# Optimization experiments

Measured on AMD Instinct MI355X. Metric: run time of the kernel, lower is better.

## Reference

```python
import jax, jax.numpy as jnp
import numpy as np

B, TQ, TK, D, F, H = 16, 256, 256, 256, 36, 8
DK = D // H          # dk = d // h
SF = int(np.sqrt(F)) # 6
MASK_VALUE = -1e30


def setup_inputs() -> dict:
    rng = jax.random.key(0)
    ks = jax.random.split(rng, 12)
    s = 0.05
    return {
        "query": jax.random.normal(ks[0], (B, TQ, D), jnp.float32),
        "key_ts": jax.random.normal(ks[1], (B, TK, D), jnp.float32),
        "value": jax.random.normal(ks[2], (B, TK, F), jnp.float32),
        "mask": (jax.random.uniform(ks[3], (B, TK, F)) < 0.5).astype(jnp.float32),
        "Wq": jax.random.normal(ks[4], (H, D, DK), jnp.float32) * s,
        "Wk": jax.random.normal(ks[5], (H, D, DK), jnp.float32) * s,
        "Wc": jax.random.normal(ks[6], (H, D), jnp.float32) * s,
        "bc": jnp.zeros((D,), jnp.float32),
        "Wo_1": jax.random.normal(ks[7], (F, SF), jnp.float32) * s,
        "bo_1": jnp.zeros((SF,), jnp.float32),
        "Wo_2": jax.random.normal(ks[8], (SF, 1), jnp.float32) * s,
        "bo_2": jnp.zeros((D,), jnp.float32),
    }


def reference(query, key_ts, value, mask, Wq, Wk, Wc, bc, Wo_1, bo_1, Wo_2, bo_2):
    # mask: [B, Tk, F] 0/1 missingness indicator -> broadcast as [B, 1, Tk, F]
    m = mask[:, None, :, :]
    heads = []
    for j in range(Wq.shape[0]):  # fixed small head loop (h=8)
        q = query @ Wq[j]                                  # [B, Tq, dk]
        k = key_ts @ Wk[j]                                 # [B, Tk, dk]
        A = jnp.einsum('bqd,bkd->bqk', q, k)[..., None]    # [B, Tq, Tk, 1] (no 1/sqrt(dk) scaling, as in original)
        A = m * A + (1.0 - m) * MASK_VALUE                 # [B, Tq, Tk, F]
        A = jax.nn.softmax(A, axis=-2)                     # softmax over Tk, per feature
        heads.append(jnp.einsum('bqkf,bkf->bqf', A, value))  # masked weighted sum
    latent = jnp.stack(heads, axis=-1)                     # [B, Tq, F, h]
    # permute (0,2,1,3) -> [B, F, Tq, h]; dot Wc[h,d] -> [B, F, Tq, d]
    latent = jnp.tanh(jnp.einsum('bqfh,hd->bfqd', latent, Wc) + bc)
    # permute (0,2,3,1) -> [B, Tq, d, F]; Wo_1: F -> sqrt(F)
    x = jnp.tanh(jnp.einsum('bfqd,fs->bqds', latent, Wo_1) + bo_1)
    # Wo_2: sqrt(F) -> 1, squeeze, add bo_2 -> [B, Tq, d]
    x = jnp.einsum('bqds,so->bqd', x, Wo_2) + bo_2
    return x
```

## Files before the change

kernel.cpp:

```cpp
#include <hip/hip_runtime.h>

#define NB 16
#define NTQ 256
#define NTK 256
#define ND 256
#define NF 36
#define NH 8
#define NDK 32
#define NSF 6

typedef __attribute__((ext_vector_type(8))) short short8;
typedef __attribute__((ext_vector_type(4))) float f32x4;
#define MFMA16(a,b,c) __builtin_amdgcn_mfma_f32_16x16x32_bf16(a,b,c,0,0,0)

#define SZ_QP  (16*8*256*32*2)
#define QPH_OFF 0
#define QPL_OFF (QPH_OFF + SZ_QP)
#define KPH_OFF (QPL_OFF + SZ_QP)
#define KPL_OFF (KPH_OFF + SZ_QP)
#define SZ_RT  (16*80*256*2)
#define RT_OFF  (KPL_OFF + SZ_QP)
#define HD_OFF  (RT_OFF + SZ_RT)

__device__ __forceinline__ short f2bf(float x){
    union { float f; unsigned u; } v; v.f = x;
    unsigned r = v.u + 0x7fffu + ((v.u >> 16) & 1u);
    return (short)(r >> 16);
}
__device__ __forceinline__ float bf2f(short s){
    union { float f; unsigned u; } v; v.u = ((unsigned)(unsigned short)s) << 16;
    return v.f;
}
__device__ __forceinline__ float fast_tanh(float x){
    float e = __expf(2.0f*x);
    return 1.0f - 2.0f/(e + 1.0f);
}
__device__ __forceinline__ short8 ld8(const short* p){ return *(const short8*)p; }

__device__ __forceinline__ void cvt8(const float* __restrict__ p, short8& h8, short8& l8){
    f32x4 a = *(const f32x4*)p;
    f32x4 c = *(const f32x4*)(p + 4);
    #pragma unroll
    for (int i = 0; i < 4; ++i){
        short h0 = f2bf(a[i]); h8[i]   = h0; l8[i]   = f2bf(a[i] - bf2f(h0));
        short h1 = f2bf(c[i]); h8[4+i] = h1; l8[4+i] = f2bf(c[i] - bf2f(h1));
    }
}

__global__ void imta_prep(const float* __restrict__ query, const float* __restrict__ key_ts,
                          const float* __restrict__ Wq, const float* __restrict__ Wk,
                          const float* __restrict__ mask, const float* __restrict__ value,
                          char* __restrict__ wsb){
    if (blockIdx.y == 2){
        const int b = blockIdx.z, k = threadIdx.x;
        short* rt = (short*)(wsb + RT_OFF) + b*80*256;
        #pragma unroll
        for (int r = 0; r < 5; ++r){
            const int fp = blockIdx.x*5 + r;
            const int f = fp >> 1;
            short o = 0;
            if (f < NF){
                float m = mask[(b*NTK + k)*NF + f];
                o = (fp & 1) ? f2bf(m) : f2bf(m * value[(b*NTK + k)*NF + f]);
            }
            rt[fp*256 + k] = o;
        }
        return;
    }
    const int side = blockIdx.y, b = blockIdx.z;
    const int mt = blockIdx.x >> 1, nh = blockIdx.x & 1;
    const int t0 = mt*32;
    const int tid = threadIdx.x, w = tid >> 6, lane = tid & 63;
    const int col = lane & 15, quad = lane >> 4;
    const float* __restrict__ X = side ? key_ts : query;
    const float* __restrict__ W = side ? Wk : Wq;
    __shared__ float sX[32][36];
    __shared__ float sW[128][36];
    const int xr = tid >> 3, xc = (tid & 7)*4;
    const int dr = tid >> 3, dkq = (tid & 7)*4;
    f32x4 acc[2][2];
    #pragma unroll
    for (int m = 0; m < 2; ++m){ acc[m][0] = (f32x4)0.f; acc[m][1] = (f32x4)0.f; }
    for (int kb = 0; kb < 8; ++kb){
        const int dc = kb*32;
        float4 xv = *(const float4*)(X + (size_t)(b*NTQ + t0 + xr)*ND + dc + xc);
        float4 wv[4];
        #pragma unroll
        for (int jj = 0; jj < 4; ++jj)
            wv[jj] = *(const float4*)(W + (size_t)((4*nh + jj)*ND + dc + dr)*NDK + dkq);
        __syncthreads();
        *(float4*)&sX[xr][xc] = xv;
        #pragma unroll
        for (int jj = 0; jj < 4; ++jj)
            #pragma unroll
            for (int i = 0; i < 4; ++i)
                sW[jj*32 + dkq + i][dr] = ((const float*)&wv[jj])[i];
        __syncthreads();
        short8 ah[2], al[2], bh[2], bl[2];
        #pragma unroll
        for (int m = 0; m < 2; ++m)
            cvt8(&sX[m*16 + col][quad*8], ah[m], al[m]);
        #pragma unroll
        for (int nt = 0; nt < 2; ++nt)
            cvt8(&sW[(w*2 + nt)*16 + col][quad*8], bh[nt], bl[nt]);
        #pragma unroll
        for (int m = 0; m < 2; ++m)
            #pragma unroll
            for (int nt = 0; nt < 2; ++nt){
                acc[m][nt] = MFMA16(al[m], bh[nt], acc[m][nt]);
                acc[m][nt] = MFMA16(ah[m], bl[nt], acc[m][nt]);
                acc[m][nt] = MFMA16(ah[m], bh[nt], acc[m][nt]);
            }
    }
    short* oh = (short*)(wsb + (side ? KPH_OFF : QPH_OFF));
    short* ol = (short*)(wsb + (side ? KPL_OFF : QPL_OFF));
    #pragma unroll
    for (int m = 0; m < 2; ++m)
        #pragma unroll
        for (int nt = 0; nt < 2; ++nt){
            const int n = (nh*8 + w*2 + nt)*16 + col;
            const int j = n >> 5, dk = n & 31;
            #pragma unroll
            for (int r = 0; r < 4; ++r){
                const int t = t0 + m*16 + quad*4 + r;
                float v = acc[m][nt][r];
                short h = f2bf(v);
                size_t o = (size_t)(((b*NH + j)*NTQ + t)*NDK + dk);
                oh[o] = h; ol[o] = f2bf(v - bf2f(h));
            }
        }
}

__global__ void imta_attn(char* __restrict__ wsb, const float* __restrict__ value){
    const int t0 = blockIdx.x*64;
    const int j = blockIdx.y, b = blockIdx.z;
    const int tid = threadIdx.x, w = tid >> 6, lane = tid & 63;
    const int col = lane & 15, quad = lane >> 4;
    __shared__ short sE[64*264];
    const short* QH = (const short*)(wsb + QPH_OFF) + (b*NH + j)*NTQ*NDK;
    const short* QL = (const short*)(wsb + QPL_OFF) + (b*NH + j)*NTQ*NDK;
    const short* KH = (const short*)(wsb + KPH_OFF) + (b*NH + j)*NTK*NDK;
    const short* KL = (const short*)(wsb + KPL_OFF) + (b*NH + j)*NTK*NDK;
    const short* RT = (const short*)(wsb + RT_OFF) + b*80*256;
    float* HD = (float*)(wsb + HD_OFF) + (b*NH + j)*NTQ*NF;

    short8 ah[4], al[4];
    #pragma unroll
    for (int m = 0; m < 4; ++m){
        const int t = t0 + m*16 + col;
        ah[m] = ld8(QH + t*NDK + quad*8);
        al[m] = ld8(QL + t*NDK + quad*8);
    }
    #pragma unroll
    for (int nt = 0; nt < 4; ++nt){
        const int key0 = w*64 + nt*16;
        short8 bh = ld8(KH + (key0 + col)*NDK + quad*8);
        short8 bl = ld8(KL + (key0 + col)*NDK + quad*8);
        f32x4 acc[4];
        #pragma unroll
        for (int m = 0; m < 4; ++m){
            f32x4 c = (f32x4)0.f;
            c = MFMA16(al[m], bh, c);
            c = MFMA16(ah[m], bl, c);
            c = MFMA16(ah[m], bh, c);
            acc[m] = c;
        }
        const int key = key0 + col;
        #pragma unroll
        for (int m = 0; m < 4; ++m)
            #pragma unroll
            for (int r = 0; r < 4; ++r){
                const int q = m*16 + quad*4 + r;
                sE[q*264 + key] = f2bf(__expf(acc[m][r]));
            }
    }
    __syncthreads();

    const int q0 = w*16;
    f32x4 acc2[5];
    #pragma unroll
    for (int nt = 0; nt < 5; ++nt) acc2[nt] = (f32x4)0.f;
    #pragma unroll 2
    for (int kb = 0; kb < 8; ++kb){
        const int ko = kb*32 + quad*8;
        short8 a = *(const short8*)&sE[(q0 + col)*264 + ko];
        #pragma unroll
        for (int nt = 0; nt < 5; ++nt){
            short8 bb = ld8(RT + (nt*16 + col)*256 + ko);
            acc2[nt] = MFMA16(a, bb, acc2[nt]);
        }
    }
    __syncthreads();
    float* sH = (float*)sE;
    #pragma unroll
    for (int nt = 0; nt < 5; ++nt)
        #pragma unroll
        for (int r = 0; r < 4; ++r){
            float v = acc2[nt][r];
            float o = __shfl_xor(v, 1, 64);
            if (!(col & 1)){
                const int f = nt*8 + (col >> 1);
                if (f < NF){
                    float num = v, den = o, h;
                    if (den != 0.0f) h = num/den;
                    else {
                        float s = 0.f;
                        for (int k = 0; k < NTK; ++k) s += value[(b*NTK + k)*NF + f];
                        h = s * (1.0f/256.0f);
                    }
                    sH[(q0 + quad*4 + r)*40 + f] = h;
                }
            }
        }
    __syncthreads();
    for (int idx = tid; idx < 64*NF; idx += 256){
        const int q = idx/NF, f = idx - q*NF;
        HD[(t0 + q)*NF + f] = sH[q*40 + f];
    }
}

__global__ void imta_final(const float* __restrict__ Wc, const float* __restrict__ bc,
                           const float* __restrict__ Wo1, const float* __restrict__ bo1,
                           const float* __restrict__ Wo2, const float* __restrict__ bo2,
                           const float* __restrict__ hd, float* __restrict__ out){
    const int bq = blockIdx.x;
    const int b = bq >> 8, qq = bq & 255;
    const int tid = threadIdx.x;
    __shared__ float sh[NF*NH];
    __shared__ float sW1[NF*NSF];
    for (int t = tid; t < NF*NH; t += 256){
        int jj = t/NF, f = t - jj*NF;
        sh[t] = hd[((b*NH + jj)*NTQ + qq)*NF + f];
    }
    if (tid < NF*NSF) sW1[tid] = Wo1[tid];
    __syncthreads();
    const int d = tid;
    float wcr[8];
    #pragma unroll
    for (int h = 0; h < 8; ++h) wcr[h] = Wc[h*ND + d];
    const float bcd = bc[d];
    float a2[6];
    #pragma unroll
    for (int s = 0; s < 6; ++s) a2[s] = bo1[s];
    #pragma unroll
    for (int f4 = 0; f4 < NF; f4 += 4){
        float4 sv[8];
        #pragma unroll
        for (int h = 0; h < 8; ++h) sv[h] = *(const float4*)&sh[h*NF + f4];
        #pragma unroll
        for (int fi = 0; fi < 4; ++fi){
            float a = bcd;
            #pragma unroll
            for (int h = 0; h < 8; ++h)
                a = fmaf(reinterpret_cast<const float*>(&sv[h])[fi], wcr[h], a);
            float lf = fast_tanh(a);
            const int f = f4 + fi;
            #pragma unroll
            for (int s = 0; s < 6; ++s)
                a2[s] = fmaf(lf, sW1[f*NSF + s], a2[s]);
        }
    }
    float o = bo2[d];
    #pragma unroll
    for (int s = 0; s < 6; ++s)
        o = fmaf(fast_tanh(a2[s]), Wo2[s], o);
    out[(b*NTQ + qq)*ND + d] = o;
}

extern "C" void kernel_launch(void* const* d_in, const int* in_sizes, int n_in,
                              void* d_out, int out_size, void* d_ws, size_t ws_size,
                              hipStream_t stream){
    const float* query  = (const float*)d_in[0];
    const float* key_ts = (const float*)d_in[1];
    const float* value  = (const float*)d_in[2];
    const float* mask   = (const float*)d_in[3];
    const float* Wq     = (const float*)d_in[4];
    const float* Wk     = (const float*)d_in[5];
    const float* Wc     = (const float*)d_in[6];
    const float* bc     = (const float*)d_in[7];
    const float* Wo1    = (const float*)d_in[8];
    const float* bo1    = (const float*)d_in[9];
    const float* Wo2    = (const float*)d_in[10];
    const float* bo2    = (const float*)d_in[11];
    char* wsb  = (char*)d_ws;
    float* out = (float*)d_out;
    (void)in_sizes; (void)n_in; (void)out_size; (void)ws_size;

    imta_prep <<<dim3(16, 3, 16), dim3(256), 0, stream>>>(query, key_ts, Wq, Wk, mask, value, wsb);
    imta_attn <<<dim3(4, 8, 16),  dim3(256), 0, stream>>>(wsb, value);
    imta_final<<<dim3(4096),      dim3(256), 0, stream>>>(Wc, bc, Wo1, bo1, Wo2, bo2,
                                                          (const float*)(wsb + HD_OFF), out);
}
```

Before: 143.0 us.

## Fuse Q/K head projections into attention kernel, prepack inputs to split-bf16

The prep kernel no longer computes the Q and K projections. It now only converts query, key_ts and the transposed Wq/Wk into hi/lo bf16 pairs, plus the mask/value RT table. Each attention block computes its own K projection for all 256 keys and the Q projection for its 64 queries with split-bf16 MFMA, staging the results in shared memory before scores. This removes the projected-Q/K round trip through global memory and the separate projection pass. The cost is that K is recomputed once per query tile (4x redundancy) and attention blocks get longer and heavier on registers.

```diff
diff --git a/kernel.cpp b/kernel.cpp
--- a/kernel.cpp
+++ b/kernel.cpp
@@ -13,14 +13,16 @@
 typedef __attribute__((ext_vector_type(4))) float f32x4;
 #define MFMA16(a,b,c) __builtin_amdgcn_mfma_f32_16x16x32_bf16(a,b,c,0,0,0)
 
-#define SZ_QP  (16*8*256*32*2)
-#define QPH_OFF 0
-#define QPL_OFF (QPH_OFF + SZ_QP)
-#define KPH_OFF (QPL_OFF + SZ_QP)
-#define KPL_OFF (KPH_OFF + SZ_QP)
-#define SZ_RT  (16*80*256*2)
-#define RT_OFF  (KPL_OFF + SZ_QP)
-#define HD_OFF  (RT_OFF + SZ_RT)
+#define QXH_OFF 0u
+#define QXL_OFF  (2u*1024*1024)
+#define KXH_OFF  (4u*1024*1024)
+#define KXL_OFF  (6u*1024*1024)
+#define WQTH_OFF (8u*1024*1024)
+#define WQTL_OFF (WQTH_OFF + 131072u)
+#define WKTH_OFF (WQTH_OFF + 262144u)
+#define WKTL_OFF (WQTH_OFF + 393216u)
+#define RT_OFF   (WQTH_OFF + 524288u)
+#define HD_OFF   (RT_OFF + 655360u)
 
 __device__ __forceinline__ short f2bf(float x){
     union { float f; unsigned u; } v; v.f = x;
@@ -47,135 +49,185 @@
     }
 }
 
-__global__ void imta_prep(const float* __restrict__ query, const float* __restrict__ key_ts,
+__global__ void imta_pack(const float* __restrict__ query, const float* __restrict__ key_ts,
                           const float* __restrict__ Wq, const float* __restrict__ Wk,
                           const float* __restrict__ mask, const float* __restrict__ value,
                           char* __restrict__ wsb){
-    if (blockIdx.y == 2){
-        const int b = blockIdx.z, k = threadIdx.x;
-        short* rt = (short*)(wsb + RT_OFF) + b*80*256;
-        #pragma unroll
-        for (int r = 0; r < 5; ++r){
-            const int fp = blockIdx.x*5 + r;
-            const int f = fp >> 1;
-            short o = 0;
-            if (f < NF){
-                float m = mask[(b*NTK + k)*NF + f];
-                o = (fp & 1) ? f2bf(m) : f2bf(m * value[(b*NTK + k)*NF + f]);
-            }
-            rt[fp*256 + k] = o;
-        }
+    const int bid = blockIdx.x, tid = threadIdx.x;
+    if (bid < 1024){
+        const int half = bid >> 9;
+        const float* __restrict__ X = half ? key_ts : query;
+        short* oh = (short*)(wsb + (half ? KXH_OFF : QXH_OFF));
+        short* ol = (short*)(wsb + (half ? KXL_OFF : QXL_OFF));
+        const int e = ((bid & 511)*256 + tid)*8;
+        short8 h8, l8;
+        cvt8(X + e, h8, l8);
+        *(short8*)(oh + e) = h8;
+        *(short8*)(ol + e) = l8;
         return;
     }
-    const int side = blockIdx.y, b = blockIdx.z;
-    const int mt = blockIdx.x >> 1, nh = blockIdx.x & 1;
-    const int t0 = mt*32;
-    const int tid = threadIdx.x, w = tid >> 6, lane = tid & 63;
-    const int col = lane & 15, quad = lane >> 4;
-    const float* __restrict__ X = side ? key_ts : query;
-    const float* __restrict__ W = side ? Wk : Wq;
-    __shared__ float sX[32][36];
-    __shared__ float sW[128][36];
-    const int xr = tid >> 3, xc = (tid & 7)*4;
-    const int dr = tid >> 3, dkq = (tid & 7)*4;
-    f32x4 acc[2][2];
-    #pragma unroll
-    for (int m = 0; m < 2; ++m){ acc[m][0] = (f32x4)0.f; acc[m][1] = (f32x4)0.f; }
-    for (int kb = 0; kb < 8; ++kb){
-        const int dc = kb*32;
-        float4 xv = *(const float4*)(X + (size_t)(b*NTQ + t0 + xr)*ND + dc + xc);
-        float4 wv[4];
-        #pragma unroll
-        for (int jj = 0; jj < 4; ++jj)
-            wv[jj] = *(const float4*)(W + (size_t)((4*nh + jj)*ND + dc + dr)*NDK + dkq);
-        __syncthreads();
-        *(float4*)&sX[xr][xc] = xv;
-        #pragma unroll
-        for (int jj = 0; jj < 4; ++jj)
-            #pragma unroll
-            for (int i = 0; i < 4; ++i)
-                sW[jj*32 + dkq + i][dr] = ((const float*)&wv[jj])[i];
-        __syncthreads();
-        short8 ah[2], al[2], bh[2], bl[2];
-        #pragma unroll
-        for (int m = 0; m < 2; ++m)
-            cvt8(&sX[m*16 + col][quad*8], ah[m], al[m]);
-        #pragma unroll
-        for (int nt = 0; nt < 2; ++nt)
-            cvt8(&sW[(w*2 + nt)*16 + col][quad*8], bh[nt], bl[nt]);
-        #pragma unroll
-        for (int m = 0; m < 2; ++m)
-            #pragma unroll
-            for (int nt = 0; nt < 2; ++nt){
-                acc[m][nt] = MFMA16(al[m], bh[nt], acc[m][nt]);
-                acc[m][nt] = MFMA16(ah[m], bl[nt], acc[m][nt]);
-                acc[m][nt] = MFMA16(ah[m], bh[nt], acc[m][nt]);
-            }
-    }
-    short* oh = (short*)(wsb + (side ? KPH_OFF : QPH_OFF));
-    short* ol = (short*)(wsb + (side ? KPL_OFF : QPL_OFF));
-    #pragma unroll
-    for (int m = 0; m < 2; ++m)
-        #pragma unroll
-        for (int nt = 0; nt < 2; ++nt){
-            const int n = (nh*8 + w*2 + nt)*16 + col;
-            const int j = n >> 5, dk = n & 31;
-            #pragma unroll
-            for (int r = 0; r < 4; ++r){
-                const int t = t0 + m*16 + quad*4 + r;
-                float v = acc[m][nt][r];
-                short h = f2bf(v);
-                size_t o = (size_t)(((b*NH + j)*NTQ + t)*NDK + dk);
-                oh[o] = h; ol[o] = f2bf(v - bf2f(h));
-            }
-        }
-}
-
-__global__ void imta_attn(char* __restrict__ wsb, const float* __restrict__ value){
+    if (bid < 1536){
+        const int idx = (bid - 1024)*256 + tid;
+        const int arr = idx >> 16, rem = idx & 65535;
+        const int d = rem & 255, jdk = rem >> 8;
+        const int jj = jdk >> 5, dk = jdk & 31;
+        const float* __restrict__ W = arr ? Wk : Wq;
+        float v = W[(jj*ND + d)*NDK + dk];
+        short h = f2bf(v);
+        short* oh = (short*)(wsb + (arr ? WKTH_OFF : WQTH_OFF));
+        short* ol = (short*)(wsb + (arr ? WKTL_OFF : WQTL_OFF));
+        oh[rem] = h; ol[rem] = f2bf(v - bf2f(h));
+        return;
+    }
+    const int rb = bid - 1536;
+    const int x = rb & 15, b = rb >> 4;
+    const int k = tid;
+    short* rt = (short*)(wsb + RT_OFF) + b*80*256;
+    #pragma unroll
+    for (int r = 0; r < 5; ++r){
+        const int fp = x*5 + r;
+        const int f = fp >> 1;
+        short o = 0;
+        if (f < NF){
+            float m = mask[(b*NTK + k)*NF + f];
+            o = (fp & 1) ? f2bf(m) : f2bf(m * value[(b*NTK + k)*NF + f]);
+        }
+        rt[fp*256 + k] = o;
+    }
+}
+
+__global__ __launch_bounds__(256, 2)
+void imta_attn(char* __restrict__ wsb, const float* __restrict__ value){
     const int t0 = blockIdx.x*64;
     const int j = blockIdx.y, b = blockIdx.z;
     const int tid = threadIdx.x, w = tid >> 6, lane = tid & 63;
     const int col = lane & 15, quad = lane >> 4;
-    __shared__ short sE[64*264];
-    const short* QH = (const short*)(wsb + QPH_OFF) + (b*NH + j)*NTQ*NDK;
-    const short* QL = (const short*)(wsb + QPL_OFF) + (b*NH + j)*NTQ*NDK;
-    const short* KH = (const short*)(wsb + KPH_OFF) + (b*NH + j)*NTK*NDK;
-    const short* KL = (const short*)(wsb + KPL_OFF) + (b*NH + j)*NTK*NDK;
-    const short* RT = (const short*)(wsb + RT_OFF) + b*80*256;
-    float* HD = (float*)(wsb + HD_OFF) + (b*NH + j)*NTQ*NF;
-
-    short8 ah[4], al[4];
-    #pragma unroll
-    for (int m = 0; m < 4; ++m){
-        const int t = t0 + m*16 + col;
-        ah[m] = ld8(QH + t*NDK + quad*8);
-        al[m] = ld8(QL + t*NDK + quad*8);
-    }
-    #pragma unroll
-    for (int nt = 0; nt < 4; ++nt){
-        const int key0 = w*64 + nt*16;
-        short8 bh = ld8(KH + (key0 + col)*NDK + quad*8);
-        short8 bl = ld8(KL + (key0 + col)*NDK + quad*8);
-        f32x4 acc[4];
+
+    __shared__ short sBuf[20480];
+    short* const sKH = sBuf;
+    short* const sKL = sBuf + 8192;
+    short* const sQH = sBuf + 16384;
+    short* const sQL = sBuf + 18432;
+
+    const short* KXH = (const short*)(wsb + KXH_OFF) + (size_t)b*NTK*ND;
+    const short* KXL = (const short*)(wsb + KXL_OFF) + (size_t)b*NTK*ND;
+    const short* QXH = (const short*)(wsb + QXH_OFF) + (size_t)b*NTQ*ND;
+    const short* QXL = (const short*)(wsb + QXL_OFF) + (size_t)b*NTQ*ND;
+    const short* WKH = (const short*)(wsb + WKTH_OFF) + j*NDK*ND;
+    const short* WKL = (const short*)(wsb + WKTL_OFF) + j*NDK*ND;
+    const short* WQH = (const short*)(wsb + WQTH_OFF) + j*NDK*ND;
+    const short* WQL = (const short*)(wsb + WQTL_OFF) + j*NDK*ND;
+
+    {
+        f32x4 kacc[4][2];
+        #pragma unroll
+        for (int mt = 0; mt < 4; ++mt){ kacc[mt][0] = (f32x4)0.f; kacc[mt][1] = (f32x4)0.f; }
+        #pragma unroll
+        for (int kb = 0; kb < 8; ++kb){
+            const int dko = kb*32 + quad*8;
+            short8 wbh[2], wbl[2];
+            #pragma unroll
+            for (int nb = 0; nb < 2; ++nb){
+                wbh[nb] = ld8(WKH + (nb*16 + col)*ND + dko);
+                wbl[nb] = ld8(WKL + (nb*16 + col)*ND + dko);
+            }
+            #pragma unroll
+            for (int mt = 0; mt < 4; ++mt){
+                const int krow = w*64 + mt*16 + col;
+                short8 ah = ld8(KXH + krow*ND + dko);
+                short8 al = ld8(KXL + krow*ND + dko);
+                #pragma unroll
+                for (int nb = 0; nb < 2; ++nb){
+                    kacc[mt][nb] = MFMA16(al, wbh[nb], kacc[mt][nb]);
+                    kacc[mt][nb] = MFMA16(ah, wbl[nb], kacc[mt][nb]);
+                    kacc[mt][nb] = MFMA16(ah, wbh[nb], kacc[mt][nb]);
+                }
+            }
+        }
+        #pragma unroll
+        for (int mt = 0; mt < 4; ++mt)
+            #pragma unroll
+            for (int nb = 0; nb < 2; ++nb)
+                #pragma unroll
+                for (int r = 0; r < 4; ++r){
+                    const int key = w*64 + mt*16 + quad*4 + r;
+                    const int dk  = nb*16 + col;
+                    float v = kacc[mt][nb][r];
+                    short h = f2bf(v);
+                    sKH[key*32 + dk] = h;
+                    sKL[key*32 + dk] = f2bf(v - bf2f(h));
+                }
+    }
+    {
+        f32x4 qacc[2]; qacc[0] = (f32x4)0.f; qacc[1] = (f32x4)0.f;
+        #pragma unroll
+        for (int kb = 0; kb < 8; ++kb){
+            const int dko = kb*32 + quad*8;
+            short8 ah = ld8(QXH + (t0 + w*16 + col)*ND + dko);
+            short8 al = ld8(QXL + (t0 + w*16 + col)*ND + dko);
+            #pragma unroll
+            for (int nb = 0; nb < 2; ++nb){
+                short8 wbh = ld8(WQH + (nb*16 + col)*ND + dko);
+                short8 wbl = ld8(WQL + (nb*16 + col)*ND + dko);
+                qacc[nb] = MFMA16(al, wbh, qacc[nb]);
+                qacc[nb] = MFMA16(ah, wbl, qacc[nb]);
+                qacc[nb] = MFMA16(ah, wbh, qacc[nb]);
+            }
+        }
+        #pragma unroll
+        for (int nb = 0; nb < 2; ++nb)
+            #pragma unroll
+            for (int r = 0; r < 4; ++r){
+                const int q  = w*16 + quad*4 + r;
+                const int dk = nb*16 + col;
+                float v = qacc[nb][r];
+                short h = f2bf(v);
+                sQH[q*32 + dk] = h;
+                sQL[q*32 + dk] = f2bf(v - bf2f(h));
+            }
+    }
+    __syncthreads();
+
+    f32x4 sacc[4][4];
+    {
+        short8 aqh[4], aql[4];
         #pragma unroll
         for (int m = 0; m < 4; ++m){
-            f32x4 c = (f32x4)0.f;
-            c = MFMA16(al[m], bh, c);
-            c = MFMA16(ah[m], bl, c);
-            c = MFMA16(ah[m], bh, c);
-            acc[m] = c;
-        }
-        const int key = key0 + col;
+            aqh[m] = *(const short8*)&sQH[(m*16 + col)*32 + quad*8];
+            aql[m] = *(const short8*)&sQL[(m*16 + col)*32 + quad*8];
+        }
+        #pragma unroll
+        for (int nt = 0; nt < 4; ++nt){
+            const int krow = w*64 + nt*16 + col;
+            short8 bh = *(const short8*)&sKH[krow*32 + quad*8];
+            short8 bl = *(const short8*)&sKL[krow*32 + quad*8];
+            #pragma unroll
+            for (int m = 0; m < 4; ++m){
+                f32x4 c = (f32x4)0.f;
+                c = MFMA16(aql[m], bh, c);
+                c = MFMA16(aqh[m], bl, c);
+                c = MFMA16(aqh[m], bh, c);
+                sacc[nt][m] = c;
+            }
+        }
+    }
+    __syncthreads();
+
+    short* const sE = sBuf;
+    #pragma unroll
+    for (int nt = 0; nt < 4; ++nt)
         #pragma unroll
         for (int m = 0; m < 4; ++m)
             #pragma unroll
             for (int r = 0; r < 4; ++r){
                 const int q = m*16 + quad*4 + r;
-                sE[q*264 + key] = f2bf(__expf(acc[m][r]));
-            }
-    }
-    __syncthreads();
-
+                const int key = w*64 + nt*16 + col;
+                sE[q*264 + key] = f2bf(__expf(sacc[nt][m][r]));
+            }
+    __syncthreads();
+
+    const short* RT = (const short*)(wsb + RT_OFF) + b*80*256;
+    float* HD = (float*)(wsb + HD_OFF) + (size_t)(b*NH + j)*NTQ*NF;
     const int q0 = w*16;
     f32x4 acc2[5];
     #pragma unroll
@@ -191,7 +243,7 @@
         }
     }
     __syncthreads();
-    float* sH = (float*)sE;
+    float* sH = (float*)sBuf;
     #pragma unroll
     for (int nt = 0; nt < 5; ++nt)
         #pragma unroll
@@ -286,8 +338,8 @@
     float* out = (float*)d_out;
     (void)in_sizes; (void)n_in; (void)out_size; (void)ws_size;
 
-    imta_prep <<<dim3(16, 3, 16), dim3(256), 0, stream>>>(query, key_ts, Wq, Wk, mask, value, wsb);
-    imta_attn <<<dim3(4, 8, 16),  dim3(256), 0, stream>>>(wsb, value);
-    imta_final<<<dim3(4096),      dim3(256), 0, stream>>>(Wc, bc, Wo1, bo1, Wo2, bo2,
-                                                          (const float*)(wsb + HD_OFF), out);
-}
+    imta_pack <<<dim3(1792),     dim3(256), 0, stream>>>(query, key_ts, Wq, Wk, mask, value, wsb);
+    imta_attn <<<dim3(4, 8, 16), dim3(256), 0, stream>>>(wsb, value);
+    imta_final<<<dim3(4096),     dim3(256), 0, stream>>>(Wc, bc, Wo1, bo1, Wo2, bo2,
+                                                         (const float*)(wsb + HD_OFF), out);
+}
```

After: 165.9 us. 1.16x slower.

## Pre-split projection weights to bf16 hi/lo and drop LDS staging in projection

Applied to the files above, without the earlier changes.

Adds a pack kernel that converts Wq/Wk once into transposed bf16 hi/lo arrays, alongside the existing mask/value packing. The projection kernel then reads the pre-split weights straight from global memory into MFMA operands, with no shared-memory staging, no __syncthreads, and no per-block weight conversion. Tiles shrink to 16 rows by 128 columns, so the grid grows. This adds one more launch, and the A-operand conversion is repeated by each column-half block. Workspace offsets are reorganised.

```diff
diff --git a/kernel.cpp b/kernel.cpp
--- a/kernel.cpp
+++ b/kernel.cpp
@@ -13,14 +13,16 @@
 typedef __attribute__((ext_vector_type(4))) float f32x4;
 #define MFMA16(a,b,c) __builtin_amdgcn_mfma_f32_16x16x32_bf16(a,b,c,0,0,0)
 
-#define SZ_QP  (16*8*256*32*2)
-#define QPH_OFF 0
-#define QPL_OFF (QPH_OFF + SZ_QP)
-#define KPH_OFF (QPL_OFF + SZ_QP)
-#define KPL_OFF (KPH_OFF + SZ_QP)
-#define SZ_RT  (16*80*256*2)
-#define RT_OFF  (KPL_OFF + SZ_QP)
-#define HD_OFF  (RT_OFF + SZ_RT)
+#define WQTH_OFF 0u
+#define WQTL_OFF (WQTH_OFF + 131072u)
+#define WKTH_OFF (WQTH_OFF + 262144u)
+#define WKTL_OFF (WQTH_OFF + 393216u)
+#define RT_OFF   (WQTH_OFF + 524288u)
+#define QPH_OFF  (2u*1024*1024)
+#define QPL_OFF  (6u*1024*1024)
+#define KPH_OFF  (10u*1024*1024)
+#define KPL_OFF  (14u*1024*1024)
+#define HD_OFF   (18u*1024*1024)
 
 __device__ __forceinline__ short f2bf(float x){
     union { float f; unsigned u; } v; v.f = x;
@@ -47,88 +49,85 @@
     }
 }
 
-__global__ void imta_prep(const float* __restrict__ query, const float* __restrict__ key_ts,
-                          const float* __restrict__ Wq, const float* __restrict__ Wk,
+__global__ void imta_pack(const float* __restrict__ Wq, const float* __restrict__ Wk,
                           const float* __restrict__ mask, const float* __restrict__ value,
                           char* __restrict__ wsb){
-    if (blockIdx.y == 2){
-        const int b = blockIdx.z, k = threadIdx.x;
-        short* rt = (short*)(wsb + RT_OFF) + b*80*256;
-        #pragma unroll
-        for (int r = 0; r < 5; ++r){
-            const int fp = blockIdx.x*5 + r;
-            const int f = fp >> 1;
-            short o = 0;
-            if (f < NF){
-                float m = mask[(b*NTK + k)*NF + f];
-                o = (fp & 1) ? f2bf(m) : f2bf(m * value[(b*NTK + k)*NF + f]);
-            }
-            rt[fp*256 + k] = o;
-        }
+    const int bid = blockIdx.x, tid = threadIdx.x;
+    if (bid < 512){
+        const int idx = bid*256 + tid;
+        const int arr = idx >> 16, rem = idx & 65535;
+        const int d = rem & 255, jdk = rem >> 8;
+        const int jj = jdk >> 5, dk = jdk & 31;
+        const float* __restrict__ W = arr ? Wk : Wq;
+        float v = W[(jj*ND + d)*NDK + dk];
+        short h = f2bf(v);
+        short* oh = (short*)(wsb + (arr ? WKTH_OFF : WQTH_OFF));
+        short* ol = (short*)(wsb + (arr ? WKTL_OFF : WQTL_OFF));
+        oh[rem] = h; ol[rem] = f2bf(v - bf2f(h));
         return;
     }
+    const int rb = bid - 512;
+    const int x = rb & 15, b = rb >> 4;
+    const int k = tid;
+    short* rt = (short*)(wsb + RT_OFF) + b*80*256;
+    #pragma unroll
+    for (int r = 0; r < 5; ++r){
+        const int fp = x*5 + r;
+        const int f = fp >> 1;
+        short o = 0;
+        if (f < NF){
+            float m = mask[(b*NTK + k)*NF + f];
+            o = (fp & 1) ? f2bf(m) : f2bf(m * value[(b*NTK + k)*NF + f]);
+        }
+        rt[fp*256 + k] = o;
+    }
+}
+
+__global__ void imta_proj(const float* __restrict__ query, const float* __restrict__ key_ts,
+                          char* __restrict__ wsb){
+    const int t0 = (blockIdx.x >> 1)*16, c0 = (blockIdx.x & 1)*128;
     const int side = blockIdx.y, b = blockIdx.z;
-    const int mt = blockIdx.x >> 1, nh = blockIdx.x & 1;
-    const int t0 = mt*32;
     const int tid = threadIdx.x, w = tid >> 6, lane = tid & 63;
     const int col = lane & 15, quad = lane >> 4;
+
     const float* __restrict__ X = side ? key_ts : query;
-    const float* __restrict__ W = side ? Wk : Wq;
-    __shared__ float sX[32][36];
-    __shared__ float sW[128][36];
-    const int xr = tid >> 3, xc = (tid & 7)*4;
-    const int dr = tid >> 3, dkq = (tid & 7)*4;
-    f32x4 acc[2][2];
-    #pragma unroll
-    for (int m = 0; m < 2; ++m){ acc[m][0] = (f32x4)0.f; acc[m][1] = (f32x4)0.f; }
+    const short* WH = (const short*)(wsb + (side ? WKTH_OFF : WQTH_OFF));
+    const short* WL = (const short*)(wsb + (side ? WKTL_OFF : WQTL_OFF));
+    short* OH = (short*)(wsb + (side ? KPH_OFF : QPH_OFF));
+    short* OL = (short*)(wsb + (side ? KPL_OFF : QPL_OFF));
+
+    const int nbase = c0 + w*32;
+    const float* xrow = X + (size_t)(b*NTQ + t0 + col)*ND;
+
+    f32x4 acc[2]; acc[0] = (f32x4)0.f; acc[1] = (f32x4)0.f;
+    #pragma unroll
     for (int kb = 0; kb < 8; ++kb){
-        const int dc = kb*32;
-        float4 xv = *(const float4*)(X + (size_t)(b*NTQ + t0 + xr)*ND + dc + xc);
-        float4 wv[4];
-        #pragma unroll
-        for (int jj = 0; jj < 4; ++jj)
-            wv[jj] = *(const float4*)(W + (size_t)((4*nh + jj)*ND + dc + dr)*NDK + dkq);
-        __syncthreads();
-        *(float4*)&sX[xr][xc] = xv;
-        #pragma unroll
-        for (int jj = 0; jj < 4; ++jj)
-            #pragma unroll
-            for (int i = 0; i < 4; ++i)
-                sW[jj*32 + dkq + i][dr] = ((const float*)&wv[jj])[i];
-        __syncthreads();
-        short8 ah[2], al[2], bh[2], bl[2];
-        #pragma unroll
-        for (int m = 0; m < 2; ++m)
-            cvt8(&sX[m*16 + col][quad*8], ah[m], al[m]);
-        #pragma unroll
-        for (int nt = 0; nt < 2; ++nt)
-            cvt8(&sW[(w*2 + nt)*16 + col][quad*8], bh[nt], bl[nt]);
-        #pragma unroll
-        for (int m = 0; m < 2; ++m)
-            #pragma unroll
-            for (int nt = 0; nt < 2; ++nt){
-                acc[m][nt] = MFMA16(al[m], bh[nt], acc[m][nt]);
-                acc[m][nt] = MFMA16(ah[m], bl[nt], acc[m][nt]);
-                acc[m][nt] = MFMA16(ah[m], bh[nt], acc[m][nt]);
-            }
-    }
-    short* oh = (short*)(wsb + (side ? KPH_OFF : QPH_OFF));
-    short* ol = (short*)(wsb + (side ? KPL_OFF : QPL_OFF));
-    #pragma unroll
-    for (int m = 0; m < 2; ++m)
+        const int dko = kb*32 + quad*8;
+        short8 ah, al;
+        cvt8(xrow + dko, ah, al);
         #pragma unroll
         for (int nt = 0; nt < 2; ++nt){
-            const int n = (nh*8 + w*2 + nt)*16 + col;
-            const int j = n >> 5, dk = n & 31;
-            #pragma unroll
-            for (int r = 0; r < 4; ++r){
-                const int t = t0 + m*16 + quad*4 + r;
-                float v = acc[m][nt][r];
-                short h = f2bf(v);
-                size_t o = (size_t)(((b*NH + j)*NTQ + t)*NDK + dk);
-                oh[o] = h; ol[o] = f2bf(v - bf2f(h));
-            }
-        }
+            const int n = nbase + nt*16 + col;
+            short8 bh = ld8(WH + n*ND + dko);
+            short8 bl = ld8(WL + n*ND + dko);
+            acc[nt] = MFMA16(al, bh, acc[nt]);
+            acc[nt] = MFMA16(ah, bl, acc[nt]);
+            acc[nt] = MFMA16(ah, bh, acc[nt]);
+        }
+    }
+    #pragma unroll
+    for (int nt = 0; nt < 2; ++nt){
+        const int n = nbase + nt*16 + col;
+        const int j = n >> 5, dk = n & 31;
+        #pragma unroll
+        for (int r = 0; r < 4; ++r){
+            const int t = t0 + quad*4 + r;
+            float v = acc[nt][r];
+            short h = f2bf(v);
+            size_t o = (size_t)(((b*NH + j)*NTQ + t)*NDK + dk);
+            OH[o] = h; OL[o] = f2bf(v - bf2f(h));
+        }
+    }
 }
 
 __global__ void imta_attn(char* __restrict__ wsb, const float* __restrict__ value){
@@ -286,8 +285,9 @@
     float* out = (float*)d_out;
     (void)in_sizes; (void)n_in; (void)out_size; (void)ws_size;
 
-    imta_prep <<<dim3(16, 3, 16), dim3(256), 0, stream>>>(query, key_ts, Wq, Wk, mask, value, wsb);
-    imta_attn <<<dim3(4, 8, 16),  dim3(256), 0, stream>>>(wsb, value);
-    imta_final<<<dim3(4096),      dim3(256), 0, stream>>>(Wc, bc, Wo1, bo1, Wo2, bo2,
-                                                          (const float*)(wsb + HD_OFF), out);
-}
+    imta_pack <<<dim3(768),      dim3(256), 0, stream>>>(Wq, Wk, mask, value, wsb);
+    imta_proj <<<dim3(32, 2, 16),dim3(256), 0, stream>>>(query, key_ts, wsb);
+    imta_attn <<<dim3(4, 8, 16), dim3(256), 0, stream>>>(wsb, value);
+    imta_final<<<dim3(4096),     dim3(256), 0, stream>>>(Wc, bc, Wo1, bo1, Wo2, bo2,
+                                                         (const float*)(wsb + HD_OFF), out);
+}
```

Result: slower. 156.2 us (+9.3%).
